# Kernel optimization log

Hardware: AMD Instinct MI355X
Metric: run time of the kernel (lower is better)

The kernel has to match this reference:

```python
import jax, jax.numpy as jnp
import numpy as np
from jax import lax

B, CIN, COUT, H, W, K, LAT = 16, 256, 256, 64, 64, 3, 512
EPS = 1e-8
LRELU_SLOPE = 0.2
ACT_GAIN = float(np.sqrt(2.0))


def setup_inputs() -> dict:
    key = jax.random.key(0)
    ks = jax.random.split(key, 6)
    # equalized-lr (implicit_lreq) init: weights already carry std = gain/sqrt(fan_in)
    conv_std = np.sqrt(2.0) / np.sqrt(CIN * K * K)   # gain=sqrt(2)
    style_std = 1.0 / np.sqrt(LAT)                    # style affine uses gain=1
    return {
        "x": jax.random.normal(ks[0], (B, CIN, H, W), jnp.float32),
        "style": jax.random.normal(ks[1], (B, LAT), jnp.float32),
        "noise": jax.random.normal(ks[2], (B, 1, H, W), jnp.float32),
        "weight": jax.random.normal(ks[3], (COUT, CIN, K, K), jnp.float32) * conv_std,
        "style_w": jax.random.normal(ks[4], (LAT, CIN), jnp.float32) * style_std,
        "style_b": jnp.ones((CIN,), jnp.float32),   # bias_initial = 1 (StyleGAN2)
        "bias": jnp.zeros((COUT,), jnp.float32),
        "noise_weight": jax.random.normal(ks[5], (1,), jnp.float32) * 0.1,
    }


def reference(x, style, noise, weight, style_w, style_b, bias, noise_weight):
    b, cin, h, w_ = x.shape
    cout = weight.shape[0]
    # style affine -> per-sample, per-input-channel modulation scales
    s = style @ style_w + style_b                              # [B, Cin]
    # modulate per-sample weights
    wmod = weight[None] * s[:, None, :, None, None]            # [B, Cout, Cin, K, K]
    # demodulate
    d = lax.rsqrt(jnp.sum(wmod * wmod, axis=(2, 3, 4)) + EPS)  # [B, Cout]
    wmod = wmod * d[:, :, None, None, None]
    # batch-as-groups conv2d
    xg = x.reshape(1, b * cin, h, w_)
    wg = wmod.reshape(b * cout, cin, K, K)
    out = lax.conv_general_dilated(
        xg, wg, window_strides=(1, 1), padding=[(1, 1), (1, 1)],
        feature_group_count=b,
        dimension_numbers=("NCHW", "OIHW", "NCHW"),
    ).reshape(b, cout, h, w_)
    # noise injection + bias + leaky relu with sqrt(2) gain
    out = out + noise * noise_weight[0] + bias[None, :, None, None]
    return jax.nn.leaky_relu(out, LRELU_SLOPE) * ACT_GAIN
```

## Files before the change

kernel.cpp:

```cpp
#include <hip/hip_runtime.h>
#include <hip/hip_bf16.h>

typedef __bf16 bf16x8 __attribute__((ext_vector_type(8)));
typedef float f32x4 __attribute__((ext_vector_type(4)));

#define LAT 512

__device__ __forceinline__ void async_load16(const void* g, void* l) {
  __builtin_amdgcn_global_load_lds(
      (const __attribute__((address_space(1))) unsigned int*)g,
      (__attribute__((address_space(3))) unsigned int*)l, 16, 0, 0);
}

__global__ void style_kernel(const float* __restrict__ style,
                             const float* __restrict__ style_w,
                             const float* __restrict__ style_b,
                             float* __restrict__ smod) {
  int b = blockIdx.x, cin = threadIdx.x;
  float acc = style_b[cin];
  const float* st = style + b * LAT;
  for (int l = 0; l < LAT; ++l)
    acc = fmaf(st[l], style_w[l * 256 + cin], acc);
  smod[b * 256 + cin] = acc;
}

__global__ void modw_kernel(const float* __restrict__ weight,
                            const float* __restrict__ smod,
                            __hip_bfloat16* __restrict__ wmod) {
  int cout = blockIdx.x, b = blockIdx.y;
  int cin = threadIdx.x;
  float s = smod[b * 256 + cin];
  const float* wp = weight + ((size_t)cout * 256 + cin) * 9;
  float w[9];
  float ss = 0.f;
#pragma unroll
  for (int j = 0; j < 9; ++j) { w[j] = wp[j]; ss = fmaf(w[j], w[j], ss); }
  ss *= s * s;
#pragma unroll
  for (int off = 32; off > 0; off >>= 1) ss += __shfl_down(ss, off, 64);
  __shared__ float red[4];
  __shared__ float dsh;
  int lane = threadIdx.x & 63, wv = threadIdx.x >> 6;
  if (lane == 0) red[wv] = ss;
  __syncthreads();
  if (threadIdx.x == 0) dsh = rsqrtf(red[0] + red[1] + red[2] + red[3] + 1e-8f);
  __syncthreads();
  float d = dsh * s;
  size_t obase = ((size_t)(b * 9) * 256 + cout) * 256 + cin;
#pragma unroll
  for (int j = 0; j < 9; ++j)
    wmod[obase + (size_t)j * 65536] = __float2bfloat16(w[j] * d);
}

__global__ void border_kernel(__hip_bfloat16* __restrict__ xt) {
  int bp = blockIdx.x;
  int b = blockIdx.y;
  int h, w;
  if (bp < 66)       { h = 0;        w = bp; }
  else if (bp < 132) { h = 65;       w = bp - 66; }
  else if (bp < 196) { h = bp - 131; w = 0; }
  else               { h = bp - 195; w = 65; }
  xt[((size_t)(b * 66 + h) * 66 + w) * 256 + threadIdx.x] = __float2bfloat16(0.f);
}

__global__ void transpose_kernel(const float* __restrict__ x,
                                 __hip_bfloat16* __restrict__ xt) {
  __shared__ __hip_bfloat16 tile[64][258];
  int h = blockIdx.x, b = blockIdx.y, t = threadIdx.x;
  int w4 = (t & 15) * 4;
  int csub = t >> 4;
  for (int c0 = 0; c0 < 256; c0 += 16) {
    int cin = c0 + csub;
    const float4 v = *(const float4*)(x + (((size_t)(b * 256 + cin) * 64 + h) << 6) + w4);
    tile[w4 + 0][cin] = __float2bfloat16(v.x);
    tile[w4 + 1][cin] = __float2bfloat16(v.y);
    tile[w4 + 2][cin] = __float2bfloat16(v.z);
    tile[w4 + 3][cin] = __float2bfloat16(v.w);
  }
  __syncthreads();
  int wsub = t >> 7;
  int cpair = t & 127;
  size_t obase = ((size_t)(b * 66 + h + 1) * 66 + 1) * 256;
  for (int w0 = 0; w0 < 64; w0 += 2) {
    int w = w0 + wsub;
    unsigned int v = *(const unsigned int*)&tile[w][cpair * 2];
    *(unsigned int*)((__hip_bfloat16*)xt + obase + (size_t)w * 256 + cpair * 2) = v;
  }
}

__global__ __launch_bounds__(256, 2)
void conv_kernel(const __hip_bfloat16* __restrict__ wmod,
                 const __hip_bfloat16* __restrict__ xt,
                 const float* __restrict__ noise,
                 const float* __restrict__ bias,
                 const float* __restrict__ nwt,
                 float* __restrict__ out) {
  __shared__ __align__(16) char lds[49152];
  const int t = threadIdx.x;

  const int bid = blockIdx.x + (blockIdx.y << 4) + (blockIdx.z << 5);
  const int nid = ((bid & 7) << 6) + (bid >> 3);
  const int sp = nid & 15;
  const int cout0 = ((nid >> 4) & 1) << 7;
  const int b = nid >> 5;

  const int lane = t & 63;
  const int wv = t >> 6;
  const int mw = (wv >> 1) << 6;
  const int nwl = (wv & 1) << 7;
  const int col = lane & 15, quad = lane >> 4;

  unsigned asrc[2];
#pragma unroll
  for (int it = 0; it < 2; ++it) {
    int ch = it * 256 + t;
    int m = ch >> 2, qs = ch & 3;
    int k8 = qs ^ ((m >> 1) & 3);
    asrc[it] = (unsigned)((cout0 + m) * 256 + k8 * 8);
  }
  const size_t wbase = (size_t)b * 9 * 65536;

  unsigned bsrc0[4];
#pragma unroll
  for (int it = 0; it < 4; ++it) {
    int ch = it * 256 + t;
    int n = ch >> 2, qs = ch & 3;
    int k8 = qs ^ ((n >> 1) & 3);
    bsrc0[it] = (unsigned)((((b * 66 + (sp << 2) + (n >> 6)) * 66 + (n & 63)) << 8) + k8 * 8);
  }

  int aro[4];
#pragma unroll
  for (int i = 0; i < 4; ++i) {
    int m = mw + i * 16 + col;
    aro[i] = (m << 6) + ((quad ^ ((m >> 1) & 3)) << 4);
  }
  int bro[8];
#pragma unroll
  for (int j = 0; j < 8; ++j) {
    int n = nwl + j * 16 + col;
    bro[j] = (n << 6) + ((quad ^ ((n >> 1) & 3)) << 4);
  }

  f32x4 acc[4][8];
#pragma unroll
  for (int i = 0; i < 4; ++i)
#pragma unroll
    for (int j = 0; j < 8; ++j)
      acc[i][j] = (f32x4){0.f, 0.f, 0.f, 0.f};

  auto stage = [&](int kc, int tap, int buf) {
    const int dtap = (tap / 3) * 66 + (tap % 3);
    const __hip_bfloat16* asrcp = wmod + wbase + tap * 65536 + kc * 32;
    const __hip_bfloat16* bsrcp = xt + (dtap << 8) + kc * 32;
    char* adst = lds + buf * 8192 + t * 16;
    char* bdst = lds + 16384 + buf * 16384 + t * 16;
    async_load16(asrcp + asrc[0], adst);
    async_load16(asrcp + asrc[1], adst + 4096);
#pragma unroll
    for (int it = 0; it < 4; ++it)
      async_load16(bsrcp + bsrc0[it], bdst + it * 4096);
  };

  auto compute = [&](int buf) {
    const char* A = lds + buf * 8192;
    const char* Bb = lds + 16384 + buf * 16384;
    bf16x8 af[4], bfr[8];
#pragma unroll
    for (int i = 0; i < 4; ++i) af[i] = *(const bf16x8*)(A + aro[i]);
#pragma unroll
    for (int j = 0; j < 8; ++j) bfr[j] = *(const bf16x8*)(Bb + bro[j]);
#pragma unroll
    for (int i = 0; i < 4; ++i)
#pragma unroll
      for (int j = 0; j < 8; ++j)
        acc[i][j] = __builtin_amdgcn_mfma_f32_16x16x32_bf16(af[i], bfr[j], acc[i][j], 0, 0, 0);
  };

  stage(0, 0, 0);
  __builtin_amdgcn_sched_barrier(0);
  stage(0, 1, 1);
  __builtin_amdgcn_sched_barrier(0);

#pragma unroll
  for (int kc = 0; kc < 8; ++kc) {
#pragma unroll
    for (int tap = 0; tap < 9; ++tap) {
      const int s = kc * 9 + tap;
      if (s == 71) asm volatile("s_waitcnt vmcnt(0)" ::: "memory");
      else         asm volatile("s_waitcnt vmcnt(6)" ::: "memory");
      __builtin_amdgcn_s_barrier();
      __builtin_amdgcn_sched_barrier(0);
      __builtin_amdgcn_s_setprio(1);
      compute(s & 1);
      __builtin_amdgcn_s_setprio(0);
      __builtin_amdgcn_s_barrier();
      __builtin_amdgcn_sched_barrier(0);
      if (s <= 69) {
        const int s2 = s + 2;
        stage(s2 / 9, s2 % 9, s & 1);
        __builtin_amdgcn_sched_barrier(0);
      }
    }
  }

  const float nw0 = nwt[0];
  float nz[8];
#pragma unroll
  for (int j = 0; j < 8; ++j)
    nz[j] = noise[(b << 12) + (sp << 8) + nwl + j * 16 + col] * nw0;
#pragma unroll
  for (int i = 0; i < 4; ++i) {
    const int mloc = mw + i * 16 + quad * 4;
    const float4 b4 = *(const float4*)(bias + cout0 + mloc);
#pragma unroll
    for (int j = 0; j < 8; ++j) {
      const int p = (sp << 8) + nwl + j * 16 + col;
      f32x4 v = acc[i][j];
      const float bb[4] = {b4.x, b4.y, b4.z, b4.w};
#pragma unroll
      for (int r = 0; r < 4; ++r) {
        const int coutg = cout0 + mloc + r;
        float val = v[r] + nz[j] + bb[r];
        val = (val > 0.f ? val : 0.2f * val) * 1.4142135623730951f;
        out[(((size_t)(b * 256 + coutg)) << 12) + p] = val;
      }
    }
  }
}

extern "C" void kernel_launch(void* const* d_in, const int* in_sizes, int n_in,
                              void* d_out, int out_size, void* d_ws, size_t ws_size,
                              hipStream_t stream) {
  const float* x        = (const float*)d_in[0];
  const float* style    = (const float*)d_in[1];
  const float* noise    = (const float*)d_in[2];
  const float* weight   = (const float*)d_in[3];
  const float* style_w  = (const float*)d_in[4];
  const float* style_b  = (const float*)d_in[5];
  const float* bias     = (const float*)d_in[6];
  const float* noise_w  = (const float*)d_in[7];
  float* out = (float*)d_out;

  char* ws = (char*)d_ws;
  float* smod = (float*)ws;
  __hip_bfloat16* wmod = (__hip_bfloat16*)(ws + 16384);
  __hip_bfloat16* xt = (__hip_bfloat16*)(ws + 16384 + 18874368);

  style_kernel<<<16, 256, 0, stream>>>(style, style_w, style_b, smod);
  modw_kernel<<<dim3(256, 16), 256, 0, stream>>>(weight, smod, wmod);
  border_kernel<<<dim3(260, 16), 256, 0, stream>>>(xt);
  transpose_kernel<<<dim3(64, 16), 256, 0, stream>>>(x, xt);
  conv_kernel<<<dim3(16, 2, 16), 256, 0, stream>>>(wmod, xt, noise, bias, noise_w, out);
}
```

Baseline: 226.7 us.

## Load weight operand directly to registers and double K-chunk per stage

The modulated-weight (A) operand no longer goes through LDS. Each wave loads its A fragments straight from global memory into double-buffered registers, one stage ahead. The B (activation) tile now covers 64 input channels per stage, with a wider XOR swizzle and a 64KB LDS buffer. This halves the number of pipeline stages and barriers. In exchange it adds redundant global A loads across waves, more VGPRs, and higher LDS use per block, which could hurt occupancy or cause spills.

```diff
diff --git a/kernel.cpp b/kernel.cpp
--- a/kernel.cpp
+++ b/kernel.cpp
@@ -95,7 +95,7 @@
                  const float* __restrict__ bias,
                  const float* __restrict__ nwt,
                  float* __restrict__ out) {
-  __shared__ __align__(16) char lds[49152];
+  __shared__ __align__(16) char lds[65536];
   const int t = threadIdx.x;
 
   const int bid = blockIdx.x + (blockIdx.y << 4) + (blockIdx.z << 5);
@@ -110,36 +110,26 @@
   const int nwl = (wv & 1) << 7;
   const int col = lane & 15, quad = lane >> 4;
 
-  unsigned asrc[2];
-#pragma unroll
-  for (int it = 0; it < 2; ++it) {
+  unsigned aoff[4];
+#pragma unroll
+  for (int i = 0; i < 4; ++i)
+    aoff[i] = (unsigned)((cout0 + mw + i * 16 + col) * 256 + quad * 8);
+  const size_t wbase = (size_t)b * 9 * 65536;
+
+  unsigned bsrc[8];
+#pragma unroll
+  for (int it = 0; it < 8; ++it) {
     int ch = it * 256 + t;
-    int m = ch >> 2, qs = ch & 3;
-    int k8 = qs ^ ((m >> 1) & 3);
-    asrc[it] = (unsigned)((cout0 + m) * 256 + k8 * 8);
-  }
-  const size_t wbase = (size_t)b * 9 * 65536;
-
-  unsigned bsrc0[4];
-#pragma unroll
-  for (int it = 0; it < 4; ++it) {
-    int ch = it * 256 + t;
-    int n = ch >> 2, qs = ch & 3;
-    int k8 = qs ^ ((n >> 1) & 3);
-    bsrc0[it] = (unsigned)((((b * 66 + (sp << 2) + (n >> 6)) * 66 + (n & 63)) << 8) + k8 * 8);
-  }
-
-  int aro[4];
-#pragma unroll
-  for (int i = 0; i < 4; ++i) {
-    int m = mw + i * 16 + col;
-    aro[i] = (m << 6) + ((quad ^ ((m >> 1) & 3)) << 4);
-  }
+    int n = ch >> 3, c8 = ch & 7;
+    int gk8 = c8 ^ (n & 7);
+    bsrc[it] = (unsigned)((((b * 66 + (sp << 2) + (n >> 6)) * 66 + (n & 63)) << 8) + gk8 * 8);
+  }
+
   int bro[8];
 #pragma unroll
   for (int j = 0; j < 8; ++j) {
     int n = nwl + j * 16 + col;
-    bro[j] = (n << 6) + ((quad ^ ((n >> 1) & 3)) << 4);
+    bro[j] = (n << 7) + ((quad ^ (n & 7)) << 4);
   }
 
   f32x4 acc[4][8];
@@ -149,58 +139,68 @@
     for (int j = 0; j < 8; ++j)
       acc[i][j] = (f32x4){0.f, 0.f, 0.f, 0.f};
 
-  auto stage = [&](int kc, int tap, int buf) {
+  bf16x8 af[2][4][2];
+
+  auto stageB = [&](int s, int buf) {
+    const int tap = s % 9, kc = s / 9;
     const int dtap = (tap / 3) * 66 + (tap % 3);
-    const __hip_bfloat16* asrcp = wmod + wbase + tap * 65536 + kc * 32;
-    const __hip_bfloat16* bsrcp = xt + (dtap << 8) + kc * 32;
-    char* adst = lds + buf * 8192 + t * 16;
-    char* bdst = lds + 16384 + buf * 16384 + t * 16;
-    async_load16(asrcp + asrc[0], adst);
-    async_load16(asrcp + asrc[1], adst + 4096);
-#pragma unroll
-    for (int it = 0; it < 4; ++it)
-      async_load16(bsrcp + bsrc0[it], bdst + it * 4096);
+    const __hip_bfloat16* src = xt + (dtap << 8) + kc * 64;
+    char* dst = lds + (buf << 15) + t * 16;
+#pragma unroll
+    for (int it = 0; it < 8; ++it)
+      async_load16(src + bsrc[it], dst + it * 4096);
   };
-
-  auto compute = [&](int buf) {
-    const char* A = lds + buf * 8192;
-    const char* Bb = lds + 16384 + buf * 16384;
-    bf16x8 af[4], bfr[8];
-#pragma unroll
-    for (int i = 0; i < 4; ++i) af[i] = *(const bf16x8*)(A + aro[i]);
-#pragma unroll
-    for (int j = 0; j < 8; ++j) bfr[j] = *(const bf16x8*)(Bb + bro[j]);
-#pragma unroll
-    for (int i = 0; i < 4; ++i)
-#pragma unroll
-      for (int j = 0; j < 8; ++j)
-        acc[i][j] = __builtin_amdgcn_mfma_f32_16x16x32_bf16(af[i], bfr[j], acc[i][j], 0, 0, 0);
+  auto loadA = [&](int s) {
+    const int tap = s % 9, kc = s / 9;
+    const __hip_bfloat16* ap = wmod + wbase + tap * 65536 + kc * 64;
+    const int pb = s & 1;
+#pragma unroll
+    for (int i = 0; i < 4; ++i) {
+      af[pb][i][0] = *(const bf16x8*)(ap + aoff[i]);
+      af[pb][i][1] = *(const bf16x8*)(ap + aoff[i] + 32);
+    }
   };
 
-  stage(0, 0, 0);
+  stageB(0, 0);
   __builtin_amdgcn_sched_barrier(0);
-  stage(0, 1, 1);
+  loadA(0);
   __builtin_amdgcn_sched_barrier(0);
-
-#pragma unroll
-  for (int kc = 0; kc < 8; ++kc) {
-#pragma unroll
-    for (int tap = 0; tap < 9; ++tap) {
-      const int s = kc * 9 + tap;
-      if (s == 71) asm volatile("s_waitcnt vmcnt(0)" ::: "memory");
-      else         asm volatile("s_waitcnt vmcnt(6)" ::: "memory");
-      __builtin_amdgcn_s_barrier();
+  stageB(1, 1);
+  __builtin_amdgcn_sched_barrier(0);
+
+#pragma unroll
+  for (int s = 0; s < 36; ++s) {
+    if (s == 35) asm volatile("s_waitcnt vmcnt(0)" ::: "memory");
+    else         asm volatile("s_waitcnt vmcnt(8)" ::: "memory");
+    __builtin_amdgcn_s_barrier();
+    __builtin_amdgcn_sched_barrier(0);
+    __builtin_amdgcn_s_setprio(1);
+    {
+      const char* Bb = lds + ((s & 1) << 15);
+#pragma unroll
+      for (int ks = 0; ks < 2; ++ks) {
+        bf16x8 bfr[8];
+#pragma unroll
+        for (int j = 0; j < 8; ++j)
+          bfr[j] = *(const bf16x8*)(Bb + (bro[j] ^ (ks << 6)));
+#pragma unroll
+        for (int i = 0; i < 4; ++i)
+#pragma unroll
+          for (int j = 0; j < 8; ++j)
+            acc[i][j] = __builtin_amdgcn_mfma_f32_16x16x32_bf16(af[s & 1][i][ks], bfr[j],
+                                                                acc[i][j], 0, 0, 0);
+      }
+    }
+    __builtin_amdgcn_s_setprio(0);
+    __builtin_amdgcn_s_barrier();
+    __builtin_amdgcn_sched_barrier(0);
+    if (s <= 34) {
+      loadA(s + 1);
       __builtin_amdgcn_sched_barrier(0);
-      __builtin_amdgcn_s_setprio(1);
-      compute(s & 1);
-      __builtin_amdgcn_s_setprio(0);
-      __builtin_amdgcn_s_barrier();
+    }
+    if (s <= 33) {
+      stageB(s + 2, s & 1);
       __builtin_amdgcn_sched_barrier(0);
-      if (s <= 69) {
-        const int s2 = s + 2;
-        stage(s2 / 9, s2 % 9, s & 1);
-        __builtin_amdgcn_sched_barrier(0);
-      }
     }
   }
 
```

Result: slower. 246.0 us (+8.5%).
